# Performance work log

Hardware: AMD Instinct MI355X
Metric: run time of the kernel (lower is better)

## Reference

```python
import jax, jax.numpy as jnp
import numpy as np

B, S, D, H = 2, 2048, 2048, 16
HD = D // H  # head_dim = 128

def _rope_tables(head_dim, context_length, theta_base=10000.0):
    inv_freq = 1.0 / theta_base ** (jnp.arange(0, head_dim, 2, dtype=jnp.float32) / head_dim)
    pos = jnp.arange(context_length, dtype=jnp.float32)
    angles = pos[:, None] * inv_freq[None, :]            # [S, HD/2]
    angles = jnp.concatenate([angles, angles], axis=1)   # [S, HD]
    return jnp.cos(angles), jnp.sin(angles)

def _apply_rope(x, cos, sin):
    # x: [b, h, s, hd]; cos/sin: [s, hd]
    hd = x.shape[-1]
    x1, x2 = x[..., : hd // 2], x[..., hd // 2 :]
    rotated = jnp.concatenate([-x2, x1], axis=-1)
    return x * cos[None, None] + rotated * sin[None, None]

def setup_inputs() -> dict:
    key = jax.random.key(0)
    ks = jax.random.split(key, 5)
    x = jax.random.normal(ks[0], (B, S, D), dtype=jnp.float32)
    scale = 1.0 / np.sqrt(D)
    Wq = jax.random.normal(ks[1], (D, D), dtype=jnp.float32) * scale
    Wk = jax.random.normal(ks[2], (D, D), dtype=jnp.float32) * scale
    Wv = jax.random.normal(ks[3], (D, D), dtype=jnp.float32) * scale
    Wo = jax.random.normal(ks[4], (D, D), dtype=jnp.float32) * scale
    cos, sin = _rope_tables(HD, S)
    return {"x": x, "Wq": Wq, "Wk": Wk, "Wv": Wv, "Wo": Wo, "cos": cos, "sin": sin}

def reference(x, Wq, Wk, Wv, Wo, cos, sin):
    b, s, _ = x.shape
    def split_heads(t):  # [b,s,D] -> [b,H,s,HD]
        return t.reshape(b, s, H, HD).transpose(0, 2, 1, 3)
    q = split_heads(x @ Wq.T)
    k = split_heads(x @ Wk.T)
    v = split_heads(x @ Wv.T)
    q = _apply_rope(q, cos[:s], sin[:s])
    k = _apply_rope(k, cos[:s], sin[:s])
    scores = jnp.einsum("bhqd,bhkd->bhqk", q, k) / np.sqrt(HD)
    causal = jnp.triu(jnp.ones((s, s), dtype=bool), k=1)
    scores = jnp.where(causal[None, None], -jnp.inf, scores)
    weights = jax.nn.softmax(scores, axis=-1)
    ctx = jnp.einsum("bhqk,bhkd->bhqd", weights, v)
    ctx = ctx.transpose(0, 2, 1, 3).reshape(b, s, D)
    return ctx @ Wo.T
```

## Files before the change

kernel.cpp:

```cpp
#include <hip/hip_runtime.h>
#include <cstdint>
#include <cmath>

#define B_ 2
#define S_ 2048
#define D_ 2048
#define H_ 16
#define HD_ 128

#define NEG_SENTINEL -1.0e30f

typedef __bf16 bf16;
typedef __attribute__((ext_vector_type(4))) __bf16 bf16x4;
typedef __attribute__((ext_vector_type(8))) __bf16 bf16x8;
typedef __attribute__((ext_vector_type(4))) float f32x4;

__device__ __forceinline__ void gload_lds16(const void* g, void* l) {
  __builtin_amdgcn_global_load_lds(
      (const __attribute__((address_space(1))) unsigned int*)g,
      (__attribute__((address_space(3))) unsigned int*)l, 16, 0, 0);
}

__device__ __forceinline__ f32x4 mfma16(bf16x8 a, bf16x8 b, f32x4 c) {
  return __builtin_amdgcn_mfma_f32_16x16x32_bf16(a, b, c, 0, 0, 0);
}

__device__ __forceinline__ void wg_barrier() {
  asm volatile("" ::: "memory");
  __builtin_amdgcn_s_barrier();
  asm volatile("" ::: "memory");
}

__global__ __launch_bounds__(256) void cvt_f32_bf16(
    const float* __restrict__ in, bf16* __restrict__ out)
{
  int i = blockIdx.x * 256 + threadIdx.x;
  f32x4 v = ((const f32x4*)in)[i];
  bf16x4 o;
#pragma unroll
  for (int j = 0; j < 4; ++j) o[j] = (bf16)v[j];
  ((bf16x4*)out)[i] = o;
}

#define GTM 128
#define GTN 128
#define GBK 64

template <typename OT>
__global__ __launch_bounds__(256) void gemm_xwt(
    const bf16* __restrict__ A, const bf16* __restrict__ W, OT* __restrict__ C,
    int M, int N, int K, int ldc)
{
  __shared__ bf16 sA[GTM * GBK];
  __shared__ bf16 sB[GTN * GBK];
  const int tid  = threadIdx.x;
  const int wave = tid >> 6, lane = tid & 63;
  const int quad = lane >> 4, l16 = lane & 15;
  const int tm = blockIdx.y * GTM;
  const int tn = blockIdx.x * GTN;
  const int wm = (wave >> 1) * 64, wn = (wave & 1) * 64;

  f32x4 acc[4][4];
#pragma unroll
  for (int i = 0; i < 4; ++i)
#pragma unroll
    for (int j = 0; j < 4; ++j) acc[i][j] = (f32x4)0.0f;

  for (int k0 = 0; k0 < K; k0 += GBK) {
    __syncthreads();
#pragma unroll
    for (int g = 0; g < 4; ++g) {
      int gb  = (g * 4 + wave) * 64;
      int p   = gb + lane;
      int row = p >> 3, pos = p & 7;
      int cc  = pos ^ (row & 7);
      gload_lds16(A + (size_t)(tm + row) * K + k0 + cc * 8, (char*)sA + (size_t)gb * 16);
      gload_lds16(W + (size_t)(tn + row) * K + k0 + cc * 8, (char*)sB + (size_t)gb * 16);
    }
    __syncthreads();

#pragma unroll
    for (int t = 0; t < 2; ++t) {
      bf16x8 af[4], bfr[4];
#pragma unroll
      for (int i = 0; i < 4; ++i) {
        int rowa = wm + i * 16 + l16;
        int posa = (t * 4 + quad) ^ (rowa & 7);
        af[i] = *(const bf16x8*)(sA + rowa * GBK + posa * 8);
        int rowb = wn + i * 16 + l16;
        int posb = (t * 4 + quad) ^ (rowb & 7);
        bfr[i] = *(const bf16x8*)(sB + rowb * GBK + posb * 8);
      }
#pragma unroll
      for (int i = 0; i < 4; ++i)
#pragma unroll
        for (int j = 0; j < 4; ++j)
          acc[i][j] = mfma16(af[i], bfr[j], acc[i][j]);
    }
  }

#pragma unroll
  for (int i = 0; i < 4; ++i)
#pragma unroll
    for (int r = 0; r < 4; ++r) {
      int row = tm + wm + i * 16 + quad * 4 + r;
#pragma unroll
      for (int j = 0; j < 4; ++j) {
        int col = tn + wn + j * 16 + l16;
        C[(size_t)row * ldc + col] = (OT)acc[i][j][r];
      }
    }
}

#define QTM 256
#define QTN 256
#define QBK 64
#define QHALF 16384
#define QBUF 65536
#define QLDS 131072

#define QSTAGE_A(kt_, h_, bi_) do { \
    char* dst_ = smem + (bi_) * QBUF + (h_) * QHALF; \
    _Pragma("unroll") \
    for (int g_ = 0; g_ < 2; ++g_) { \
      int p_   = g_ * 512 + tid; \
      int row_ = p_ >> 3; \
      int cc_  = (p_ & 7) ^ (row_ & 7); \
      gload_lds16(A + (size_t)(tm + (h_) * 128 + row_) * K + (size_t)(kt_) * QBK + cc_ * 8, \
                  dst_ + (size_t)p_ * 16); \
    } } while (0)

#define QSTAGE_B(kt_, h_, bi_) do { \
    char* dst_ = smem + (bi_) * QBUF + 32768 + (h_) * QHALF; \
    _Pragma("unroll") \
    for (int g_ = 0; g_ < 2; ++g_) { \
      int p_   = g_ * 512 + tid; \
      int row_ = p_ >> 3; \
      int cc_  = (p_ & 7) ^ (row_ & 7); \
      gload_lds16(W + (size_t)(tn + (h_) * 128 + row_) * K + (size_t)(kt_) * QBK + cc_ * 8, \
                  dst_ + (size_t)p_ * 16); \
    } } while (0)

#define QREAD_A(Ab_, rh_) \
    _Pragma("unroll") \
    for (int i_ = 0; i_ < 4; ++i_) \
    _Pragma("unroll") \
    for (int t2_ = 0; t2_ < 2; ++t2_) { \
      int rr_ = (rh_) * 64 + i_ * 16 + l16; \
      int ps_ = (t2_ * 4 + quad) ^ (rr_ & 7); \
      a[i_][t2_] = *(const bf16x8*)((Ab_) + rr_ * 64 + ps_ * 8); \
    }

#define QREAD_B(Bb_, bv_, ch_) \
    _Pragma("unroll") \
    for (int j_ = 0; j_ < 2; ++j_) \
    _Pragma("unroll") \
    for (int t2_ = 0; t2_ < 2; ++t2_) { \
      int rb_ = wn64 + (ch_) * 32 + j_ * 16 + l16; \
      int ps_ = (t2_ * 4 + quad) ^ (rb_ & 7); \
      bv_[j_][t2_] = *(const bf16x8*)((Bb_) + rb_ * 64 + ps_ * 8); \
    }

#define QMFMA(rh_, ch_, bv_) \
    __builtin_amdgcn_s_setprio(1); \
    _Pragma("unroll") \
    for (int i_ = 0; i_ < 4; ++i_) \
    _Pragma("unroll") \
    for (int j_ = 0; j_ < 2; ++j_) \
    _Pragma("unroll") \
    for (int t2_ = 0; t2_ < 2; ++t2_) \
      acc[(rh_) * 4 + i_][(ch_) * 2 + j_] = \
          mfma16(a[i_][t2_], bv_[j_][t2_], acc[(rh_) * 4 + i_][(ch_) * 2 + j_]); \
    __builtin_amdgcn_s_setprio(0);

#define LGK0()  asm volatile("s_waitcnt lgkmcnt(0)" ::: "memory")
#define LGK8()  asm volatile("s_waitcnt lgkmcnt(8)" ::: "memory")
#define VM4()   asm volatile("s_waitcnt vmcnt(4)" ::: "memory")
#define VM0()   asm volatile("s_waitcnt vmcnt(0)" ::: "memory")

__global__ __launch_bounds__(512, 2) void gemm_8ph(
    const bf16* __restrict__ A, const bf16* __restrict__ W, bf16* __restrict__ C,
    int M, int N, int K, int ldc, int nby)
{
  extern __shared__ char smem[];
  const int tid  = threadIdx.x;
  const int wave = tid >> 6, lane = tid & 63;
  const int quad = lane >> 4, l16 = lane & 15;

  const int nwg = (int)gridDim.x;
  const int cpx = nwg >> 3;
  const int wg  = ((int)blockIdx.x & 7) * cpx + ((int)blockIdx.x >> 3);
  const int bx = wg / nby, by = wg % nby;
  const int tm = by * QTM, tn = bx * QTN;
  const int wm = (wave >> 2) * 128;
  const int wn = (wave & 3) * 64;
  const int wn64 = wn & 64;

  const bf16* A0 = (const bf16*)(smem + (wm >> 7) * QHALF);
  const bf16* B0 = (const bf16*)(smem + 32768 + (wn >> 7) * QHALF);
  const bf16* A1 = (const bf16*)(smem + QBUF + (wm >> 7) * QHALF);
  const bf16* B1 = (const bf16*)(smem + QBUF + 32768 + (wn >> 7) * QHALF);

  const int NT = K / QBK;
  const int NI = NT >> 1;

  f32x4 acc[8][4];
#pragma unroll
  for (int i = 0; i < 8; ++i)
#pragma unroll
    for (int j = 0; j < 4; ++j) acc[i][j] = (f32x4)0.0f;

  bf16x8 a[4][2], b0[2][2], b1[2][2];

  QSTAGE_A(0, 0, 0);
  QSTAGE_A(0, 1, 0);
  QSTAGE_B(0, 0, 0);
  QSTAGE_B(0, 1, 0);
  QSTAGE_B(1, 0, 1);
  QSTAGE_B(1, 1, 1);
  VM4();
  wg_barrier();

#pragma unroll 1
  for (int it = 0; it < NI; ++it) {
    const int t0 = it * 2, t1 = t0 + 1;
    const bool last = (it == NI - 1);

    QREAD_A(A0, 0);
    QREAD_B(B0, b0, 0);
    QSTAGE_A(t1, 0, 1);
    LGK8();
    wg_barrier();
    LGK0();
    QMFMA(0, 0, b0);
    wg_barrier();

    QREAD_B(B0, b1, 1);
    QSTAGE_A(t1, 1, 1);
    wg_barrier();
    LGK0();
    QMFMA(0, 1, b1);
    wg_barrier();

    QREAD_A(A0, 1);
    if (!last) QSTAGE_B(t0 + 2, 0, 0);
    wg_barrier();
    LGK0();
    QMFMA(1, 1, b1);
    wg_barrier();

    if (!last) QSTAGE_B(t0 + 2, 1, 0);
    wg_barrier();
    QMFMA(1, 0, b0);
    if (last) { VM0(); } else { VM4(); }
    wg_barrier();

    QREAD_A(A1, 0);
    QREAD_B(B1, b0, 0);
    if (!last) QSTAGE_A(t0 + 2, 0, 0);
    LGK8();
    wg_barrier();
    LGK0();
    QMFMA(0, 0, b0);
    wg_barrier();

    QREAD_B(B1, b1, 1);
    if (!last) QSTAGE_A(t0 + 2, 1, 0);
    wg_barrier();
    LGK0();
    QMFMA(0, 1, b1);
    wg_barrier();

    QREAD_A(A1, 1);
    if (!last) QSTAGE_B(t1 + 2, 0, 1);
    wg_barrier();
    LGK0();
    QMFMA(1, 1, b1);
    wg_barrier();

    if (!last) QSTAGE_B(t1 + 2, 1, 1);
    wg_barrier();
    QMFMA(1, 0, b0);
    if (!last) { VM4(); }
    wg_barrier();
  }

#pragma unroll
  for (int ii = 0; ii < 8; ++ii)
#pragma unroll
    for (int r = 0; r < 4; ++r) {
      int row = tm + wm + (ii >> 2) * 64 + (ii & 3) * 16 + quad * 4 + r;
#pragma unroll
      for (int jj = 0; jj < 4; ++jj) {
        int col = tn + wn + jj * 16 + l16;
        C[(size_t)row * ldc + col] = (bf16)acc[ii][jj][r];
      }
    }
}

__global__ __launch_bounds__(256) void rope_qk(
    bf16* __restrict__ Q, bf16* __restrict__ Kk,
    const float* __restrict__ cosT, const float* __restrict__ sinT, int rs)
{
  const float kappa = 0.08838834764831845f * 1.4426950408889634f;
  int t = blockIdx.x * 256 + threadIdx.x;
  int d = t & 63;
  int h = (t >> 6) & (H_ - 1);
  int s = (t >> 10) & (S_ - 1);
  int b = t >> 21;
  size_t base = ((size_t)(b * S_ + s)) * rs + (size_t)h * HD_;
  float c1 = cosT[s * HD_ + d];
  float s1 = sinT[s * HD_ + d];
  float c2 = cosT[s * HD_ + d + 64];
  float s2 = sinT[s * HD_ + d + 64];
  {
    float x1 = (float)Q[base + d], x2 = (float)Q[base + d + 64];
    Q[base + d]      = (bf16)((x1 * c1 - x2 * s1) * kappa);
    Q[base + d + 64] = (bf16)((x2 * c2 + x1 * s2) * kappa);
  }
  {
    float x1 = (float)Kk[base + d], x2 = (float)Kk[base + d + 64];
    Kk[base + d]      = (bf16)(x1 * c1 - x2 * s1);
    Kk[base + d + 64] = (bf16)(x2 * c2 + x1 * s2);
  }
}

__global__ __launch_bounds__(256) void transpose_v(
    const bf16* __restrict__ V, bf16* __restrict__ Vt, int rs)
{
  __shared__ bf16 sT[64 * 72];
  const int tid = threadIdx.x;
  const int si = blockIdx.x;
  const int di = blockIdx.y;
  const int bh = blockIdx.z;
  const int b  = bh >> 4, h = bh & 15;

  const bf16* src = V + (size_t)b * S_ * rs + (size_t)h * HD_ + di * 64;
  bf16*       dst = Vt + ((size_t)bh * HD_ + di * 64) * S_ + si * 64;

#pragma unroll
  for (int half = 0; half < 2; ++half) {
    int r  = half * 32 + (tid >> 3);
    int c0 = (tid & 7) * 8;
    bf16x8 v = *(const bf16x8*)(src + (size_t)(si * 64 + r) * rs + c0);
    *(bf16x8*)(sT + r * 72 + c0) = v;
  }
  __syncthreads();
#pragma unroll
  for (int half = 0; half < 2; ++half) {
    int dr = half * 32 + (tid >> 3);
    int c0 = (tid & 7) * 8;
    bf16x8 o;
#pragma unroll
    for (int j = 0; j < 8; ++j) o[j] = sT[(c0 + j) * 72 + dr];
    *(bf16x8*)(dst + (size_t)dr * S_ + c0) = o;
  }
}

#define ABK 64
#define SPS 72

__global__ __launch_bounds__(256) void attn_fwd(
    const bf16* __restrict__ Q, const bf16* __restrict__ K,
    const bf16* __restrict__ Vt, bf16* __restrict__ O, int rs)
{
  __shared__ bf16 sK[ABK * HD_];
  __shared__ bf16 sVT[HD_ * ABK];
  __shared__ bf16 sP[64 * SPS];

  const int tid  = threadIdx.x;
  const int wave = tid >> 6, lane = tid & 63;
  const int quad = lane >> 4, l16 = lane & 15;

  const int lin   = (int)blockIdx.x;
  const int low3  = lin & 7;
  const int rest  = lin >> 3;
  const int pairx = rest & 15;
  const int colhi = rest >> 4;
  const int col   = low3 + (colhi << 3);
  const int b = col >> 4, h = col & 15;

  const bf16* Qh  = Q + (size_t)b * S_ * rs + (size_t)h * HD_;
  const bf16* Kh  = K + (size_t)b * S_ * rs + (size_t)h * HD_;
  const bf16* Vth = Vt + ((size_t)(b * H_ + h) * HD_) * S_;
  bf16*       Oh  = O + (size_t)b * S_ * D_ + (size_t)h * HD_;

  const int wq = wave * 16;

#pragma unroll 1
  for (int seg = 0; seg < 2; ++seg) {
    const int qt = seg == 0 ? pairx : 31 - pairx;
    const int q0 = qt * 64;
    const int wq_abs = q0 + wq;

    bf16x8 qf[4];
    {
      const bf16* rp = Qh + (size_t)(wq_abs + l16) * rs + quad * 8;
#pragma unroll
      for (int t = 0; t < 4; ++t) qf[t] = *(const bf16x8*)(rp + t * 32);
    }

    f32x4 o_acc[8];
#pragma unroll
    for (int j = 0; j < 8; ++j) o_acc[j] = (f32x4)0.0f;
    float m_col = NEG_SENTINEL;
    float l_col = 0.0f;

    const int nkt = qt + 1;
#pragma unroll 1
    for (int kt = 0; kt < nkt; ++kt) {
      const int kk0 = kt * ABK;
      __syncthreads();

#pragma unroll
      for (int g = 0; g < 4; ++g) {
        int p   = g * 256 + tid;
        int row = p >> 4, pos = p & 15;
        int cc  = pos ^ (row & 15);
        gload_lds16(Kh + (size_t)(kk0 + row) * rs + cc * 8, (char*)sK + (size_t)p * 16);
      }
#pragma unroll
      for (int g = 0; g < 4; ++g) {
        int p  = g * 256 + tid;
        int d  = p >> 3, pos = p & 7;
        int cc = pos ^ (d & 7);
        gload_lds16(Vth + (size_t)d * S_ + kk0 + cc * 8, (char*)sVT + (size_t)p * 16);
      }
      __syncthreads();

      if (kk0 <= wq_abs + 15) {
        f32x4 st[4];
#pragma unroll
        for (int jt = 0; jt < 4; ++jt) {
          bf16x8 kf[4];
#pragma unroll
          for (int t = 0; t < 4; ++t) {
            int pos = (t * 4 + quad) ^ l16;
            kf[t] = *(const bf16x8*)(sK + (jt * 16 + l16) * HD_ + pos * 8);
          }
          f32x4 a2 = (f32x4)0.0f;
#pragma unroll
          for (int t = 0; t < 4; ++t) a2 = mfma16(kf[t], qf[t], a2);
          st[jt] = a2;
        }

        if (kk0 + 63 > wq_abs) {
          int qcol = wq_abs + l16;
#pragma unroll
          for (int jt = 0; jt < 4; ++jt)
#pragma unroll
            for (int r = 0; r < 4; ++r) {
              int key = kk0 + jt * 16 + quad * 4 + r;
              if (key > qcol) st[jt][r] = NEG_SENTINEL;
            }
        }

        float mx = NEG_SENTINEL;
#pragma unroll
        for (int jt = 0; jt < 4; ++jt)
#pragma unroll
          for (int r = 0; r < 4; ++r) mx = fmaxf(mx, st[jt][r]);
        mx = fmaxf(mx, __shfl_xor(mx, 16, 64));
        mx = fmaxf(mx, __shfl_xor(mx, 32, 64));
        float m_new = fmaxf(m_col, mx);
        float alpha = exp2f(m_col - m_new);
        float ts = 0.0f;
#pragma unroll
        for (int jt = 0; jt < 4; ++jt) {
          bf16x4 pk;
#pragma unroll
          for (int r = 0; r < 4; ++r) {
            float p = exp2f(st[jt][r] - m_new);
            ts += p;
            pk[r] = (bf16)p;
          }
          *(bf16x4*)(sP + (wq + l16) * SPS + jt * 16 + quad * 4) = pk;
        }
        ts += __shfl_xor(ts, 16, 64);
        ts += __shfl_xor(ts, 32, 64);
        l_col = l_col * alpha + ts;
        m_col = m_new;
#pragma unroll
        for (int r = 0; r < 4; ++r) {
          float av = __shfl(alpha, quad * 4 + r, 64);
#pragma unroll
          for (int jd = 0; jd < 8; ++jd) o_acc[jd][r] *= av;
        }

#pragma unroll
        for (int ks = 0; ks < 2; ++ks) {
          bf16x8 pf = *(const bf16x8*)(sP + (wq + l16) * SPS + ks * 32 + quad * 8);
#pragma unroll
          for (int jd = 0; jd < 8; ++jd) {
            int pos = (ks * 4 + quad) ^ (l16 & 7);
            bf16x8 vf = *(const bf16x8*)(sVT + (jd * 16 + l16) * ABK + pos * 8);
            o_acc[jd] = mfma16(pf, vf, o_acc[jd]);
          }
        }
      }
    }

#pragma unroll
    for (int r = 0; r < 4; ++r) {
      float lv = __shfl(l_col, quad * 4 + r, 64);
      float inv_l = 1.0f / lv;
      int row = wq_abs + quad * 4 + r;
#pragma unroll
      for (int jd = 0; jd < 8; ++jd) {
        int colo = jd * 16 + l16;
        Oh[(size_t)row * D_ + colo] = (bf16)(o_acc[jd][r] * inv_l);
      }
    }
  }
}

extern "C" void kernel_launch(void* const* d_in, const int* in_sizes, int n_in,
                              void* d_out, int out_size, void* d_ws, size_t ws_size,
                              hipStream_t stream) {
  const float* x    = (const float*)d_in[0];
  const float* Wq   = (const float*)d_in[1];
  const float* Wk   = (const float*)d_in[2];
  const float* Wv   = (const float*)d_in[3];
  const float* Wo   = (const float*)d_in[4];
  const float* cosT = (const float*)d_in[5];
  const float* sinT = (const float*)d_in[6];
  float* out = (float*)d_out;

  const size_t NE = (size_t)B_ * S_ * D_;
  const size_t WE = (size_t)D_ * D_;
  const int M = B_ * S_;
  const int cvtX = (int)(NE / 1024);
  const int cvtW = (int)(WE / 1024);

  static bool attr_done = false;
  if (!attr_done) {
    (void)hipFuncSetAttribute(reinterpret_cast<const void*>(gemm_8ph),
                              hipFuncAttributeMaxDynamicSharedMemorySize, QLDS);
    attr_done = true;
  }

  if (ws_size >= (size_t)92274688) {
    bf16* QKV   = (bf16*)d_ws;
    bf16* xb    = QKV + (size_t)M * 6144;
    bf16* Wqkv  = xb + NE;
    bf16* ctx   = Wqkv;
    bf16* Wob   = Wqkv + 2 * WE;
    bf16* Vt    = xb;

    cvt_f32_bf16<<<cvtX, 256, 0, stream>>>(x, xb);
    cvt_f32_bf16<<<cvtW, 256, 0, stream>>>(Wq, Wqkv);
    cvt_f32_bf16<<<cvtW, 256, 0, stream>>>(Wk, Wqkv + WE);
    cvt_f32_bf16<<<cvtW, 256, 0, stream>>>(Wv, Wqkv + 2 * WE);
    gemm_8ph<<<384, 512, QLDS, stream>>>(xb, Wqkv, QKV, M, 3 * D_, D_, 3 * D_, 16);
    rope_qk<<<(B_ * S_ * H_ * 64) / 256, 256, 0, stream>>>(QKV, QKV + D_, cosT, sinT, 3 * D_);
    transpose_v<<<dim3(32, 2, 32), 256, 0, stream>>>(QKV + 2 * D_, Vt, 3 * D_);
    attn_fwd<<<512, 256, 0, stream>>>(QKV, QKV + D_, Vt, ctx, 3 * D_);
    cvt_f32_bf16<<<cvtW, 256, 0, stream>>>(Wo, Wob);
    gemm_xwt<float><<<dim3(16, 32), 256, 0, stream>>>(ctx, Wob, out, M, D_, D_, D_);
  } else {
    bf16* Qb    = (bf16*)d_ws;
    bf16* Kb    = Qb + NE;
    bf16* Vb    = Kb + NE;
    bf16* Cb    = Vb + NE;
    bf16* Wslot = Cb + NE;

    cvt_f32_bf16<<<cvtX, 256, 0, stream>>>(x, Cb);
    cvt_f32_bf16<<<cvtW, 256, 0, stream>>>(Wq, Wslot);
    gemm_xwt<bf16><<<dim3(16, 32), 256, 0, stream>>>(Cb, Wslot, Qb, M, D_, D_, D_);
    cvt_f32_bf16<<<cvtW, 256, 0, stream>>>(Wk, Wslot);
    gemm_xwt<bf16><<<dim3(16, 32), 256, 0, stream>>>(Cb, Wslot, Kb, M, D_, D_, D_);
    cvt_f32_bf16<<<cvtW, 256, 0, stream>>>(Wv, Wslot);
    gemm_xwt<bf16><<<dim3(16, 32), 256, 0, stream>>>(Cb, Wslot, Vb, M, D_, D_, D_);
    rope_qk<<<(B_ * S_ * H_ * 64) / 256, 256, 0, stream>>>(Qb, Kb, cosT, sinT, D_);
    transpose_v<<<dim3(32, 2, 32), 256, 0, stream>>>(Vb, Cb, D_);
    attn_fwd<<<512, 256, 0, stream>>>(Qb, Kb, Cb, Vb, D_);
    cvt_f32_bf16<<<cvtW, 256, 0, stream>>>(Wo, Wslot);
    gemm_xwt<float><<<dim3(16, 32), 256, 0, stream>>>(Vb, Wslot, out, M, D_, D_, D_);
  }
}
```

Measured before the change: 399.6 us.

## Double-buffer attention K/V tiles, vectorize RoPE, fuse conversions, split QKV GEMM

The attention kernel now runs 512 threads over 128-query tiles and double-buffers its K and V^T LDS tiles, so the next tile's global-to-LDS load overlaps compute on the current one. RoPE now processes 8 elements per thread with 16-byte vector loads and stores. The four conversion launches are merged into one kernel. The QKV projection is split: gemm_8ph computes Q and K over 256 blocks and gemm_xwt computes V. These changes cut launch overhead and load stalls, but double the LDS footprint and halve the attention grid, which may reduce occupancy.

Result: faster. 384.0 us (-3.9%).

```diff
diff --git a/kernel.cpp b/kernel.cpp
--- a/kernel.cpp
+++ b/kernel.cpp
@@ -30,6 +30,8 @@
   __builtin_amdgcn_s_barrier();
   asm volatile("" ::: "memory");
 }
+
+#define AVM0() asm volatile("s_waitcnt vmcnt(0)" ::: "memory")
 
 __global__ __launch_bounds__(256) void cvt_f32_bf16(
     const float* __restrict__ in, bf16* __restrict__ out)
@@ -39,6 +41,28 @@
   bf16x4 o;
 #pragma unroll
   for (int j = 0; j < 4; ++j) o[j] = (bf16)v[j];
+  ((bf16x4*)out)[i] = o;
+}
+
+__global__ __launch_bounds__(256) void cvt_qkvx(
+    const float* __restrict__ x, bf16* __restrict__ xb,
+    const float* __restrict__ wq, const float* __restrict__ wk,
+    const float* __restrict__ wv, bf16* __restrict__ wout)
+{
+  int b = (int)blockIdx.x;
+  const float* in; bf16* out; int base;
+  if (b < 8192)      { in = x;  out = xb; base = b; }
+  else {
+    int r = b - 8192; int j = r >> 12; base = r & 4095;
+    if (j == 0)      { in = wq; out = wout; }
+    else if (j == 1) { in = wk; out = wout + 4194304; }
+    else             { in = wv; out = wout + 8388608; }
+  }
+  int i = base * 256 + threadIdx.x;
+  f32x4 v = ((const f32x4*)in)[i];
+  bf16x4 o;
+#pragma unroll
+  for (int t2 = 0; t2 < 4; ++t2) o[t2] = (bf16)v[t2];
   ((bf16x4*)out)[i] = o;
 }
 
@@ -303,26 +327,37 @@
     const float* __restrict__ cosT, const float* __restrict__ sinT, int rs)
 {
   const float kappa = 0.08838834764831845f * 1.4426950408889634f;
-  int t = blockIdx.x * 256 + threadIdx.x;
-  int d = t & 63;
-  int h = (t >> 6) & (H_ - 1);
-  int s = (t >> 10) & (S_ - 1);
-  int b = t >> 21;
+  int t  = blockIdx.x * 256 + threadIdx.x;
+  int d0 = (t & 7) * 8;
+  int h  = (t >> 3) & (H_ - 1);
+  int s  = (t >> 7) & (S_ - 1);
+  int b  = t >> 18;
   size_t base = ((size_t)(b * S_ + s)) * rs + (size_t)h * HD_;
-  float c1 = cosT[s * HD_ + d];
-  float s1 = sinT[s * HD_ + d];
-  float c2 = cosT[s * HD_ + d + 64];
-  float s2 = sinT[s * HD_ + d + 64];
-  {
-    float x1 = (float)Q[base + d], x2 = (float)Q[base + d + 64];
-    Q[base + d]      = (bf16)((x1 * c1 - x2 * s1) * kappa);
-    Q[base + d + 64] = (bf16)((x2 * c2 + x1 * s2) * kappa);
-  }
-  {
-    float x1 = (float)Kk[base + d], x2 = (float)Kk[base + d + 64];
-    Kk[base + d]      = (bf16)(x1 * c1 - x2 * s1);
-    Kk[base + d + 64] = (bf16)(x2 * c2 + x1 * s2);
-  }
+
+  const float* cl = cosT + s * HD_ + d0;
+  const float* sl = sinT + s * HD_ + d0;
+
+  bf16x8 ql = *(const bf16x8*)(Q + base + d0);
+  bf16x8 qh = *(const bf16x8*)(Q + base + 64 + d0);
+  bf16x8 kl = *(const bf16x8*)(Kk + base + d0);
+  bf16x8 kh = *(const bf16x8*)(Kk + base + 64 + d0);
+
+  bf16x8 qlo, qho, klo, kho;
+#pragma unroll
+  for (int i = 0; i < 8; ++i) {
+    float c1 = cl[i], s1 = sl[i];
+    float c2 = cl[64 + i], s2 = sl[64 + i];
+    float x1 = (float)ql[i], x2 = (float)qh[i];
+    qlo[i] = (bf16)((x1 * c1 - x2 * s1) * kappa);
+    qho[i] = (bf16)((x2 * c2 + x1 * s2) * kappa);
+    float y1 = (float)kl[i], y2 = (float)kh[i];
+    klo[i] = (bf16)(y1 * c1 - y2 * s1);
+    kho[i] = (bf16)(y2 * c2 + y1 * s2);
+  }
+  *(bf16x8*)(Q + base + d0)       = qlo;
+  *(bf16x8*)(Q + base + 64 + d0)  = qho;
+  *(bf16x8*)(Kk + base + d0)      = klo;
+  *(bf16x8*)(Kk + base + 64 + d0) = kho;
 }
 
 __global__ __launch_bounds__(256) void transpose_v(
@@ -360,13 +395,35 @@
 #define ABK 64
 #define SPS 72
 
-__global__ __launch_bounds__(256) void attn_fwd(
+#define AK_STAGE(kt_, b_) do { \
+    int kk_ = (kt_) * ABK; \
+    _Pragma("unroll") \
+    for (int g_ = 0; g_ < 2; ++g_) { \
+      int p_   = g_ * 512 + tid; \
+      int row_ = p_ >> 4, pos_ = p_ & 15; \
+      int cc_  = pos_ ^ (row_ & 15); \
+      gload_lds16(Kh + (size_t)(kk_ + row_) * rs + cc_ * 8, \
+                  (char*)sK + (b_) * 16384 + (size_t)p_ * 16); \
+    } } while (0)
+
+#define AV_STAGE(kt_, b_) do { \
+    int kk_ = (kt_) * ABK; \
+    _Pragma("unroll") \
+    for (int g_ = 0; g_ < 2; ++g_) { \
+      int p_  = g_ * 512 + tid; \
+      int d_  = p_ >> 3, pos_ = p_ & 7; \
+      int cc_ = pos_ ^ (d_ & 7); \
+      gload_lds16(Vth + (size_t)d_ * S_ + kk_ + cc_ * 8, \
+                  (char*)sVT + (b_) * 16384 + (size_t)p_ * 16); \
+    } } while (0)
+
+__global__ __launch_bounds__(512) void attn_fwd(
     const bf16* __restrict__ Q, const bf16* __restrict__ K,
     const bf16* __restrict__ Vt, bf16* __restrict__ O, int rs)
 {
-  __shared__ bf16 sK[ABK * HD_];
-  __shared__ bf16 sVT[HD_ * ABK];
-  __shared__ bf16 sP[64 * SPS];
+  __shared__ bf16 sK[2 * ABK * HD_];
+  __shared__ bf16 sVT[2 * HD_ * ABK];
+  __shared__ bf16 sP[128 * SPS];
 
   const int tid  = threadIdx.x;
   const int wave = tid >> 6, lane = tid & 63;
@@ -375,8 +432,8 @@
   const int lin   = (int)blockIdx.x;
   const int low3  = lin & 7;
   const int rest  = lin >> 3;
-  const int pairx = rest & 15;
-  const int colhi = rest >> 4;
+  const int pairx = rest & 7;
+  const int colhi = rest >> 3;
   const int col   = low3 + (colhi << 3);
   const int b = col >> 4, h = col & 15;
 
@@ -389,8 +446,8 @@
 
 #pragma unroll 1
   for (int seg = 0; seg < 2; ++seg) {
-    const int qt = seg == 0 ? pairx : 31 - pairx;
-    const int q0 = qt * 64;
+    const int qt = seg == 0 ? pairx : 15 - pairx;
+    const int q0 = qt * 128;
     const int wq_abs = q0 + wq;
 
     bf16x8 qf[4];
@@ -406,27 +463,24 @@
     float m_col = NEG_SENTINEL;
     float l_col = 0.0f;
 
-    const int nkt = qt + 1;
+    const int nkt = 2 * qt + 2;
+
+    AK_STAGE(0, 0);
+    AV_STAGE(0, 0);
+    AVM0();
+    wg_barrier();
+
+    int cur = 0;
 #pragma unroll 1
     for (int kt = 0; kt < nkt; ++kt) {
       const int kk0 = kt * ABK;
-      __syncthreads();
-
-#pragma unroll
-      for (int g = 0; g < 4; ++g) {
-        int p   = g * 256 + tid;
-        int row = p >> 4, pos = p & 15;
-        int cc  = pos ^ (row & 15);
-        gload_lds16(Kh + (size_t)(kk0 + row) * rs + cc * 8, (char*)sK + (size_t)p * 16);
+      const bf16* sKc = sK + cur * (ABK * HD_);
+      const bf16* sVc = sVT + cur * (HD_ * ABK);
+
+      if (kt + 1 < nkt) {
+        AK_STAGE(kt + 1, cur ^ 1);
+        AV_STAGE(kt + 1, cur ^ 1);
       }
-#pragma unroll
-      for (int g = 0; g < 4; ++g) {
-        int p  = g * 256 + tid;
-        int d  = p >> 3, pos = p & 7;
-        int cc = pos ^ (d & 7);
-        gload_lds16(Vth + (size_t)d * S_ + kk0 + cc * 8, (char*)sVT + (size_t)p * 16);
-      }
-      __syncthreads();
 
       if (kk0 <= wq_abs + 15) {
         f32x4 st[4];
@@ -436,7 +490,7 @@
 #pragma unroll
           for (int t = 0; t < 4; ++t) {
             int pos = (t * 4 + quad) ^ l16;
-            kf[t] = *(const bf16x8*)(sK + (jt * 16 + l16) * HD_ + pos * 8);
+            kf[t] = *(const bf16x8*)(sKc + (jt * 16 + l16) * HD_ + pos * 8);
           }
           f32x4 a2 = (f32x4)0.0f;
 #pragma unroll
@@ -493,11 +547,15 @@
 #pragma unroll
           for (int jd = 0; jd < 8; ++jd) {
             int pos = (ks * 4 + quad) ^ (l16 & 7);
-            bf16x8 vf = *(const bf16x8*)(sVT + (jd * 16 + l16) * ABK + pos * 8);
+            bf16x8 vf = *(const bf16x8*)(sVc + (jd * 16 + l16) * ABK + pos * 8);
             o_acc[jd] = mfma16(pf, vf, o_acc[jd]);
           }
         }
       }
+
+      AVM0();
+      wg_barrier();
+      cur ^= 1;
     }
 
 #pragma unroll
@@ -531,6 +589,7 @@
   const int M = B_ * S_;
   const int cvtX = (int)(NE / 1024);
   const int cvtW = (int)(WE / 1024);
+  const int ropeG = (B_ * S_ * H_ * 8) / 256;
 
   static bool attr_done = false;
   if (!attr_done) {
@@ -547,14 +606,12 @@
     bf16* Wob   = Wqkv + 2 * WE;
     bf16* Vt    = xb;
 
-    cvt_f32_bf16<<<cvtX, 256, 0, stream>>>(x, xb);
-    cvt_f32_bf16<<<cvtW, 256, 0, stream>>>(Wq, Wqkv);
-    cvt_f32_bf16<<<cvtW, 256, 0, stream>>>(Wk, Wqkv + WE);
-    cvt_f32_bf16<<<cvtW, 256, 0, stream>>>(Wv, Wqkv + 2 * WE);
-    gemm_8ph<<<384, 512, QLDS, stream>>>(xb, Wqkv, QKV, M, 3 * D_, D_, 3 * D_, 16);
-    rope_qk<<<(B_ * S_ * H_ * 64) / 256, 256, 0, stream>>>(QKV, QKV + D_, cosT, sinT, 3 * D_);
+    cvt_qkvx<<<8192 + 3 * 4096, 256, 0, stream>>>(x, xb, Wq, Wk, Wv, Wqkv);
+    gemm_8ph<<<256, 512, QLDS, stream>>>(xb, Wqkv, QKV, M, 4096, D_, 3 * D_, 16);
+    gemm_xwt<bf16><<<dim3(16, 32), 256, 0, stream>>>(xb, Wqkv + 2 * WE, QKV + 4096, M, D_, D_, 3 * D_);
+    rope_qk<<<ropeG, 256, 0, stream>>>(QKV, QKV + D_, cosT, sinT, 3 * D_);
     transpose_v<<<dim3(32, 2, 32), 256, 0, stream>>>(QKV + 2 * D_, Vt, 3 * D_);
-    attn_fwd<<<512, 256, 0, stream>>>(QKV, QKV + D_, Vt, ctx, 3 * D_);
+    attn_fwd<<<256, 512, 0, stream>>>(QKV, QKV + D_, Vt, ctx, 3 * D_);
     cvt_f32_bf16<<<cvtW, 256, 0, stream>>>(Wo, Wob);
     gemm_xwt<float><<<dim3(16, 32), 256, 0, stream>>>(ctx, Wob, out, M, D_, D_, D_);
   } else {
@@ -571,9 +628,9 @@
     gemm_xwt<bf16><<<dim3(16, 32), 256, 0, stream>>>(Cb, Wslot, Kb, M, D_, D_, D_);
     cvt_f32_bf16<<<cvtW, 256, 0, stream>>>(Wv, Wslot);
     gemm_xwt<bf16><<<dim3(16, 32), 256, 0, stream>>>(Cb, Wslot, Vb, M, D_, D_, D_);
-    rope_qk<<<(B_ * S_ * H_ * 64) / 256, 256, 0, stream>>>(Qb, Kb, cosT, sinT, D_);
+    rope_qk<<<ropeG, 256, 0, stream>>>(Qb, Kb, cosT, sinT, D_);
     transpose_v<<<dim3(32, 2, 32), 256, 0, stream>>>(Vb, Cb, D_);
-    attn_fwd<<<512, 256, 0, stream>>>(Qb, Kb, Cb, Vb, D_);
+    attn_fwd<<<256, 512, 0, stream>>>(Qb, Kb, Cb, Vb, D_);
     cvt_f32_bf16<<<cvtW, 256, 0, stream>>>(Wo, Wslot);
     gemm_xwt<float><<<dim3(16, 32), 256, 0, stream>>>(Vb, Wslot, out, M, D_, D_, D_);
   }
```
